# Kernel optimization log

Hardware: AMD Instinct MI355X
Metric: run time of the kernel (lower is better)

## Reference

```python
import jax, jax.numpy as jnp
import numpy as np
from jax import lax

NEG = -1e30  # finite stand-in for -inf (identical math through softmax/logaddexp, safe grads)


def _ctc_loss_sum(log_probs, labels, input_lens, label_lens, blank=0):
    """CTC negative log-likelihood, summed over batch (torch.nn.CTCLoss reduction='sum').
    log_probs: (T, B, V) log-softmaxed; labels: (B, L) int; lens: (B,) int."""
    T, B, V = log_probs.shape
    L = labels.shape[1]
    S = 2 * L + 1
    # extended label sequence with interleaved blanks: (B, S)
    ext = jnp.full((B, S), blank, dtype=labels.dtype).at[:, 1::2].set(labels)
    prev2 = jnp.concatenate([jnp.full((B, 2), blank, dtype=ext.dtype), ext[:, :-2]], axis=1)
    skip = (ext != blank) & (ext != prev2) & (jnp.arange(S)[None, :] >= 2)  # (B, S)
    # gather per-frame log-probs of extended labels: (T, B, S)
    lp_ext = log_probs[:, jnp.arange(B)[:, None], ext]
    alpha0 = jnp.full((B, S), NEG, log_probs.dtype)
    alpha0 = alpha0.at[:, 0].set(lp_ext[0, :, 0]).at[:, 1].set(lp_ext[0, :, 1])
    pad1 = jnp.full((B, 1), NEG, log_probs.dtype)
    pad2 = jnp.full((B, 2), NEG, log_probs.dtype)

    def step(alpha, inp):
        lp_t, t = inp
        a1 = jnp.concatenate([pad1, alpha[:, :-1]], axis=1)
        a2 = jnp.where(skip, jnp.concatenate([pad2, alpha[:, :-2]], axis=1), NEG)
        new = jnp.logaddexp(jnp.logaddexp(alpha, a1), a2) + lp_t
        new = jnp.where((t < input_lens)[:, None], new, alpha)  # freeze past each seq end
        return new, None

    alpha, _ = lax.scan(step, alpha0, (lp_ext[1:], jnp.arange(1, T)))
    bidx = jnp.arange(B)
    ll = jnp.logaddexp(alpha[bidx, 2 * label_lens - 1], alpha[bidx, 2 * label_lens])
    return -jnp.sum(ll)


def setup_inputs() -> dict:
    key = jax.random.key(0)
    k1, k2, k3 = jax.random.split(key, 3)
    B, T, D, V, L = 16, 1024, 512, 5000, 64
    hs_pad = jax.random.normal(k1, (B, T, D), dtype=jnp.float32)
    W = jax.random.normal(k2, (D, V), dtype=jnp.float32) * 0.02
    b = jnp.zeros((V,), dtype=jnp.float32)
    hlens = jnp.full((B,), T, dtype=jnp.int32)
    ys_pad = jax.random.randint(k3, (B, L), 1, V, dtype=jnp.int64)  # avoid blank id 0
    ys_lens = jnp.full((B,), L, dtype=jnp.int32)
    return {"hs_pad": hs_pad, "W": W, "b": b, "hlens": hlens, "ys_pad": ys_pad, "ys_lens": ys_lens}


def reference(hs_pad, W, b, hlens, ys_pad, ys_lens):
    B, T, D = hs_pad.shape
    V = W.shape[1]
    # ctc_lo projection (dropout_rate = 0.0 -> identity dropout)
    logits = jnp.einsum('btd,dv->btv', hs_pad, W) + b  # (B, T, V)
    # scatter-based mask: only classes appearing in ys_pad[b] plus ids {0,1} stay live
    allowed = jnp.zeros((B, V), dtype=bool)
    allowed = allowed.at[jnp.arange(B)[:, None], ys_pad].set(True).at[:, :2].set(True)
    logits = jnp.where(allowed[:, None, :], logits, NEG)  # masked_fill(-inf)
    log_probs = jax.nn.log_softmax(logits, axis=-1).transpose(1, 0, 2)  # (T, B, V)
    loss = _ctc_loss_sum(log_probs, ys_pad, hlens, ys_lens) / B
    return loss
```

## Files before the change

kernel.cpp:

```cpp
#include <hip/hip_runtime.h>
#include <hip/hip_bf16.h>
#include <cstdint>

#define NEGV -1e30f

constexpr int B = 16, T = 1024, D = 512, V = 5000, L = 64;
constexpr int NJ = 66;
constexpr int NJP = 80;
#define LOG2E 1.4426950408889634f
#define LN2   0.6931471805599453f
#define PSH   6.0f

typedef __attribute__((ext_vector_type(8))) short bf16x8;
typedef __attribute__((ext_vector_type(4))) int   i32x4;
typedef __attribute__((ext_vector_type(4))) float f32x4;

template <int CTRL>
__device__ __forceinline__ float dppf(float x) {
    return __int_as_float(__builtin_amdgcn_update_dpp(
        __float_as_int(x), __float_as_int(x), CTRL, 0xf, 0xf, false));
}
__device__ __forceinline__ float shup1(float x, float fill) {
    int r = __builtin_amdgcn_update_dpp(__float_as_int(fill), __float_as_int(x),
                                        0x138, 0xf, 0xf, false);
    return __int_as_float(r);
}
__device__ __forceinline__ float wmax64(float x) {
    x = fmaxf(x, dppf<0x111>(x));
    x = fmaxf(x, dppf<0x112>(x));
    x = fmaxf(x, dppf<0x114>(x));
    x = fmaxf(x, dppf<0x118>(x));
    x = fmaxf(x, dppf<0x142>(x));
    x = fmaxf(x, dppf<0x143>(x));
    return __int_as_float(__builtin_amdgcn_readlane(__float_as_int(x), 63));
}
__device__ __forceinline__ void ctc_step2(float& aA, float& aB, float& aE,
        float p_b, float p_l, float cpl) {
    float pA = shup1(aA, 0.f);
    float pB = shup1(aB, 0.f);
    float tS = aA + aB;
    float tA = aA * p_b;
    float tE = aE * p_b;
    float tP = pA * cpl;
    float nA = fmaf(pB, p_b, tA);
    float nB = fmaf(tS, p_l, tP);
    float nE = fmaf(aB, p_b, tE);
    aA = nA; aB = nB; aE = nE;
}
__device__ __forceinline__ void ctc_step2_g(float& aA, float& aB, float& aE,
        float p_b, float p_l, float cpl, bool upd) {
    float pA = shup1(aA, 0.f);
    float pB = shup1(aB, 0.f);
    float tS = aA + aB;
    float tA = aA * p_b;
    float tE = aE * p_b;
    float tP = pA * cpl;
    float nA = fmaf(pB, p_b, tA);
    float nB = fmaf(tS, p_l, tP);
    float nE = fmaf(aB, p_b, tE);
    if (upd) { aA = nA; aB = nB; aE = nE; }
}
__device__ __forceinline__ void renorm(float& x0, float& x1, float& x2, int& Esum) {
    float m = wmax64(fmaxf(fmaxf(x0, x1), x2));
    int e = ((__float_as_int(m) >> 23) & 255) - 127;
    float sc = __int_as_float((127 - e) << 23);
    x0 *= sc; x1 *= sc; x2 *= sc; Esum += e;
}
__device__ __forceinline__ int pk2(float lo, float hi) {
    return (int)((__float_as_uint(hi) & 0xFFFF0000u) | (__float_as_uint(lo) >> 16));
}

__global__ __launch_bounds__(256) void k_gather(const float* __restrict__ W,
        const float* __restrict__ bias, const int* __restrict__ ys,
        short* __restrict__ WgtT, float* __restrict__ biasG,
        unsigned* __restrict__ foMask) {
    int b = blockIdx.x, c = blockIdx.y, tid = threadIdx.x;
    __shared__ int cls[NJP];
    __shared__ unsigned mw[3];
    if (tid < NJP) cls[tid] = (tid < 2) ? tid : (tid < NJ ? ys[b * L + tid - 2] : 0);
    if (tid < 3) mw[tid] = 0u;
    __syncthreads();
    if (c == 0) {
        if (tid < NJ) {
            bool first = true;
            for (int k = 0; k < tid; ++k) if (cls[k] == cls[tid]) { first = false; break; }
            if (first) atomicOr(&mw[tid >> 5], 1u << (tid & 31));
        }
        __syncthreads();
        if (tid < 3) foMask[b * 4 + tid] = mw[tid];
        if (tid == 3) foMask[b * 4 + 3] = 0u;
        if (tid < NJP) biasG[b * NJP + tid] = (tid < NJ) ? bias[cls[tid]] : 0.f;
    }
    int kt = tid & 63, jg = tid >> 6;
    for (int j = jg; j < NJP; j += 4) {
        int d = c * 64 + kt;
        float v = (j < NJ) ? W[(size_t)d * V + cls[j]] : 0.f;
        WgtT[((size_t)b * NJP + j) * D + d] = (short)(__float_as_uint(v) >> 16);
    }
}

__global__ __launch_bounds__(64) void k_scores(const float* __restrict__ hs,
        const short* __restrict__ WgtT, const float* __restrict__ biasG,
        const unsigned* __restrict__ foMask,
        float* __restrict__ lpb, float* __restrict__ lplT) {
    int b = blockIdx.y, t0 = blockIdx.x * 16;
    int lane = threadIdx.x, cl = lane & 15, kg = lane >> 4;

    f32x4 acc[5];
    const float* __restrict__ bg = biasG + b * NJP;
    #pragma unroll
    for (int nt = 0; nt < 5; ++nt) {
        float bv = bg[nt * 16 + cl];
        acc[nt] = (f32x4){bv, bv, bv, bv};
    }

    const float* __restrict__ arow = hs + ((size_t)(b * T) + t0 + cl) * D + kg * 8;
    const short* __restrict__ brow = WgtT + ((size_t)b * NJP + cl) * D + kg * 8;

    #pragma unroll 4
    for (int ks = 0; ks < 16; ++ks) {
        int k0 = ks * 32;
        float4 a0 = *(const float4*)(arow + k0);
        float4 a1 = *(const float4*)(arow + k0 + 4);
        i32x4 ap = { pk2(a0.x, a0.y), pk2(a0.z, a0.w),
                     pk2(a1.x, a1.y), pk2(a1.z, a1.w) };
        bf16x8 af = __builtin_bit_cast(bf16x8, ap);
        #pragma unroll
        for (int nt = 0; nt < 5; ++nt) {
            bf16x8 bf = *(const bf16x8*)(brow + (size_t)nt * 16 * D + k0);
            acc[nt] = __builtin_amdgcn_mfma_f32_16x16x32_bf16(af, bf, acc[nt], 0, 0, 0);
        }
    }

    unsigned m0 = foMask[b * 4 + 0], m1 = foMask[b * 4 + 1], m2 = foMask[b * 4 + 2];
    bool on[5];
    on[0] = (m0 >> cl) & 1;        on[1] = (m0 >> (16 + cl)) & 1;
    on[2] = (m1 >> cl) & 1;        on[3] = (m1 >> (16 + cl)) & 1;
    on[4] = (cl < 2) ? ((m2 >> cl) & 1) : false;

    float lse[4];
    #pragma unroll
    for (int r = 0; r < 4; ++r) {
        float mx = NEGV;
        #pragma unroll
        for (int nt = 0; nt < 5; ++nt) if (on[nt]) mx = fmaxf(mx, acc[nt][r]);
        mx = fmaxf(mx, __shfl_xor(mx, 1));
        mx = fmaxf(mx, __shfl_xor(mx, 2));
        mx = fmaxf(mx, __shfl_xor(mx, 4));
        mx = fmaxf(mx, __shfl_xor(mx, 8));
        float s = 0.f;
        #pragma unroll
        for (int nt = 0; nt < 5; ++nt) if (on[nt]) s += __expf(acc[nt][r] - mx);
        s += __shfl_xor(s, 1);
        s += __shfl_xor(s, 2);
        s += __shfl_xor(s, 4);
        s += __shfl_xor(s, 8);
        lse[r] = mx + __logf(s);
    }

    __shared__ float Pt2[64][20];
    __shared__ float Pb[16];
    #pragma unroll
    for (int nt = 0; nt < 5; ++nt) {
        int col = nt * 16 + cl;
        #pragma unroll
        for (int r = 0; r < 4; ++r) {
            int t = kg * 4 + r;
            float pv = exp2f((acc[nt][r] - lse[r]) * LOG2E + PSH);
            if (col == 0) Pb[t] = pv;
            else if (col >= 2 && col < NJ) Pt2[col - 2][t] = pv;
        }
    }
    __syncthreads();
    float* __restrict__ orow = lplT + (size_t)b * 64 * T + (size_t)lane * T + t0;
    #pragma unroll
    for (int i = 0; i < 4; ++i)
        *(float4*)(orow + 4 * i) = *(const float4*)&Pt2[lane][4 * i];
    if (lane < 4) {
        float4 v = make_float4(Pb[4*lane], Pb[4*lane+1], Pb[4*lane+2], Pb[4*lane+3]);
        *(float4*)(lpb + b * T + t0 + 4 * lane) = v;
    }
}

__global__ __launch_bounds__(64) void k_ctc(const float* __restrict__ lpb,
        const float* __restrict__ lplT, const int* __restrict__ ys,
        const int* __restrict__ hlens, const int* __restrict__ yslens,
        float* __restrict__ ll) {
    int b = blockIdx.x, l = threadIdx.x;
    int lab = ys[b * L + l];
    int labm1 = __shfl_up(lab, 1);
    float skm = ((l >= 1) && (lab != 0) && (lab != labm1)) ? 1.0f : 0.0f;
    int hlen = hlens[b];
    int s2 = 2 * yslens[b];
    const float* __restrict__ lpbb = lpb + b * T;
    const float* __restrict__ lpt  = lplT + (size_t)b * 64 * T + (size_t)l * T;

    float aA = (l == 0) ? lpbb[0] : 0.f;
    float aB = (l == 0) ? lpt[0]  : 0.f;
    float aE = 0.f;
    int Esum = 0;

    float prl[15], prb[15];
    #pragma unroll
    for (int u = 0; u < 15; ++u) { prl[u] = lpt[1 + u]; prb[u] = lpbb[1 + u]; }
    float4 curl[4], curb[4], midl[4], midb[4], farl[4], farb[4];
    #pragma unroll
    for (int i = 0; i < 4; ++i) {
        curl[i] = *(const float4*)(lpt  + 16 + 4 * i);
        curb[i] = *(const float4*)(lpbb + 16 + 4 * i);
        midl[i] = *(const float4*)(lpt  + 32 + 4 * i);
        midb[i] = *(const float4*)(lpbb + 32 + 4 * i);
    }

    #pragma unroll
    for (int u = 0; u < 15; ++u) {
        int t = 1 + u;
        ctc_step2_g(aA, aB, aE, prb[u], prl[u], skm * prl[u], t < hlen);
    }
    renorm(aA, aB, aE, Esum);

    for (int g = 1; g < 64; ++g) {
        int t0 = 16 * g;
        if (g < 62) {
            const float* sl = lpt  + t0 + 32;
            const float* sb = lpbb + t0 + 32;
            #pragma unroll
            for (int i = 0; i < 4; ++i) {
                farl[i] = *(const float4*)(sl + 4 * i);
                farb[i] = *(const float4*)(sb + 4 * i);
            }
        }
        float pl[16], pb[16], cp[16];
        #pragma unroll
        for (int i = 0; i < 4; ++i) {
            pl[4*i+0] = curl[i].x; pl[4*i+1] = curl[i].y;
            pl[4*i+2] = curl[i].z; pl[4*i+3] = curl[i].w;
            pb[4*i+0] = curb[i].x; pb[4*i+1] = curb[i].y;
            pb[4*i+2] = curb[i].z; pb[4*i+3] = curb[i].w;
        }
        #pragma unroll
        for (int u = 0; u < 16; ++u) cp[u] = skm * pl[u];
        if (t0 + 16 <= hlen) {
            #pragma unroll
            for (int u = 0; u < 16; ++u)
                ctc_step2(aA, aB, aE, pb[u], pl[u], cp[u]);
        } else {
            #pragma unroll
            for (int u = 0; u < 16; ++u) {
                int t = t0 + u;
                ctc_step2_g(aA, aB, aE, pb[u], pl[u], cp[u], t < hlen);
            }
        }
        if ((g & 1) == 0 || g == 63) renorm(aA, aB, aE, Esum);
        #pragma unroll
        for (int i = 0; i < 4; ++i) {
            curl[i] = midl[i]; midl[i] = farl[i];
            curb[i] = midb[i]; midb[i] = farb[i];
        }
    }

    int s1 = s2 - 1;
    float v1 = __shfl(aB, s1 >> 1);
    float v2 = (s2 >= 2 * L) ? __shfl(aE, 63) : __shfl(aA, s2 >> 1);
    if (l == 0)
        ll[b] = LN2 * (__log2f(v1 + v2) + (float)Esum - PSH * (float)hlen);
}

__global__ void k_final(const float* __restrict__ ll, float* __restrict__ out) {
    if (threadIdx.x == 0 && blockIdx.x == 0) {
        float s = 0.f;
        for (int i = 0; i < B; ++i) s += ll[i];
        out[0] = -s / (float)B;
    }
}

extern "C" void kernel_launch(void* const* d_in, const int* in_sizes, int n_in,
                              void* d_out, int out_size, void* d_ws, size_t ws_size,
                              hipStream_t stream) {
    const float* hs    = (const float*)d_in[0];
    const float* W     = (const float*)d_in[1];
    const float* bias  = (const float*)d_in[2];
    const int*  hlens  = (const int*)d_in[3];
    const int*  ys     = (const int*)d_in[4];
    const int*  yslens = (const int*)d_in[5];

    char* ws = (char*)d_ws;
    unsigned* foMask = (unsigned*)(ws);
    float* biasG = (float*)(ws + 256);
    short* WgtT  = (short*)(ws + 5376);
    float* lpb   = (float*)(ws + 1316096);
    float* lplT  = (float*)(ws + 1381632);
    float* ll    = (float*)(ws + 5575936);

    hipLaunchKernelGGL(k_gather, dim3(B, 8), dim3(256), 0, stream,
                       W, bias, ys, WgtT, biasG, foMask);
    hipLaunchKernelGGL(k_scores, dim3(T / 16, B), dim3(64), 0, stream,
                       hs, WgtT, biasG, foMask, lpb, lplT);
    hipLaunchKernelGGL(k_ctc, dim3(B), dim3(64), 0, stream,
                       lpb, lplT, ys, hlens, yslens, ll);
    hipLaunchKernelGGL(k_final, dim3(1), dim3(64), 0, stream, ll, (float*)d_out);
}
```

Measured before the change: 88.93 us.

## Double k_scores time tile to reuse B fragments and fold final reduction into atomics

k_scores now handles 32 time steps per block using two accumulator sets, so each loaded bf16 weight fragment feeds two MFMAs and the grid is halved. Separately, the k_final launch is removed: k_gather zeroes the output and k_ctc atomically adds each batch's scaled loss. This cuts weight-load traffic and one kernel launch, but doubles register pressure in k_scores, leaves fewer blocks to fill the GPU, and makes the sum order nondeterministic.

```diff
diff --git a/kernel.cpp b/kernel.cpp
--- a/kernel.cpp
+++ b/kernel.cpp
@@ -73,8 +73,9 @@
 __global__ __launch_bounds__(256) void k_gather(const float* __restrict__ W,
         const float* __restrict__ bias, const int* __restrict__ ys,
         short* __restrict__ WgtT, float* __restrict__ biasG,
-        unsigned* __restrict__ foMask) {
+        unsigned* __restrict__ foMask, float* __restrict__ out) {
     int b = blockIdx.x, c = blockIdx.y, tid = threadIdx.x;
+    if (b == 0 && c == 0 && tid == 0) out[0] = 0.f;
     __shared__ int cls[NJP];
     __shared__ unsigned mw[3];
     if (tid < NJP) cls[tid] = (tid < 2) ? tid : (tid < NJ ? ys[b * L + tid - 2] : 0);
@@ -103,32 +104,40 @@
         const short* __restrict__ WgtT, const float* __restrict__ biasG,
         const unsigned* __restrict__ foMask,
         float* __restrict__ lpb, float* __restrict__ lplT) {
-    int b = blockIdx.y, t0 = blockIdx.x * 16;
+    int b = blockIdx.y, t0 = blockIdx.x * 32;
     int lane = threadIdx.x, cl = lane & 15, kg = lane >> 4;
 
-    f32x4 acc[5];
+    f32x4 acc0[5], acc1[5];
     const float* __restrict__ bg = biasG + b * NJP;
     #pragma unroll
     for (int nt = 0; nt < 5; ++nt) {
         float bv = bg[nt * 16 + cl];
-        acc[nt] = (f32x4){bv, bv, bv, bv};
-    }
-
-    const float* __restrict__ arow = hs + ((size_t)(b * T) + t0 + cl) * D + kg * 8;
+        acc0[nt] = (f32x4){bv, bv, bv, bv};
+        acc1[nt] = (f32x4){bv, bv, bv, bv};
+    }
+
+    const float* __restrict__ arow0 = hs + ((size_t)(b * T) + t0 + cl) * D + kg * 8;
+    const float* __restrict__ arow1 = arow0 + (size_t)16 * D;
     const short* __restrict__ brow = WgtT + ((size_t)b * NJP + cl) * D + kg * 8;
 
     #pragma unroll 4
     for (int ks = 0; ks < 16; ++ks) {
         int k0 = ks * 32;
-        float4 a0 = *(const float4*)(arow + k0);
-        float4 a1 = *(const float4*)(arow + k0 + 4);
-        i32x4 ap = { pk2(a0.x, a0.y), pk2(a0.z, a0.w),
-                     pk2(a1.x, a1.y), pk2(a1.z, a1.w) };
-        bf16x8 af = __builtin_bit_cast(bf16x8, ap);
+        float4 a0 = *(const float4*)(arow0 + k0);
+        float4 a1 = *(const float4*)(arow0 + k0 + 4);
+        float4 a2 = *(const float4*)(arow1 + k0);
+        float4 a3 = *(const float4*)(arow1 + k0 + 4);
+        i32x4 ap0 = { pk2(a0.x, a0.y), pk2(a0.z, a0.w),
+                      pk2(a1.x, a1.y), pk2(a1.z, a1.w) };
+        i32x4 ap1 = { pk2(a2.x, a2.y), pk2(a2.z, a2.w),
+                      pk2(a3.x, a3.y), pk2(a3.z, a3.w) };
+        bf16x8 af0 = __builtin_bit_cast(bf16x8, ap0);
+        bf16x8 af1 = __builtin_bit_cast(bf16x8, ap1);
         #pragma unroll
         for (int nt = 0; nt < 5; ++nt) {
             bf16x8 bf = *(const bf16x8*)(brow + (size_t)nt * 16 * D + k0);
-            acc[nt] = __builtin_amdgcn_mfma_f32_16x16x32_bf16(af, bf, acc[nt], 0, 0, 0);
+            acc0[nt] = __builtin_amdgcn_mfma_f32_16x16x32_bf16(af0, bf, acc0[nt], 0, 0, 0);
+            acc1[nt] = __builtin_amdgcn_mfma_f32_16x16x32_bf16(af1, bf, acc1[nt], 0, 0, 0);
         }
     }
 
@@ -138,45 +147,56 @@
     on[2] = (m1 >> cl) & 1;        on[3] = (m1 >> (16 + cl)) & 1;
     on[4] = (cl < 2) ? ((m2 >> cl) & 1) : false;
 
-    float lse[4];
+    float lse0[4], lse1[4];
     #pragma unroll
     for (int r = 0; r < 4; ++r) {
-        float mx = NEGV;
-        #pragma unroll
-        for (int nt = 0; nt < 5; ++nt) if (on[nt]) mx = fmaxf(mx, acc[nt][r]);
-        mx = fmaxf(mx, __shfl_xor(mx, 1));
-        mx = fmaxf(mx, __shfl_xor(mx, 2));
-        mx = fmaxf(mx, __shfl_xor(mx, 4));
-        mx = fmaxf(mx, __shfl_xor(mx, 8));
-        float s = 0.f;
-        #pragma unroll
-        for (int nt = 0; nt < 5; ++nt) if (on[nt]) s += __expf(acc[nt][r] - mx);
-        s += __shfl_xor(s, 1);
-        s += __shfl_xor(s, 2);
-        s += __shfl_xor(s, 4);
-        s += __shfl_xor(s, 8);
-        lse[r] = mx + __logf(s);
-    }
-
-    __shared__ float Pt2[64][20];
-    __shared__ float Pb[16];
+        float mxa = NEGV, mxb = NEGV;
+        #pragma unroll
+        for (int nt = 0; nt < 5; ++nt) if (on[nt]) {
+            mxa = fmaxf(mxa, acc0[nt][r]);
+            mxb = fmaxf(mxb, acc1[nt][r]);
+        }
+        mxa = fmaxf(mxa, __shfl_xor(mxa, 1)); mxb = fmaxf(mxb, __shfl_xor(mxb, 1));
+        mxa = fmaxf(mxa, __shfl_xor(mxa, 2)); mxb = fmaxf(mxb, __shfl_xor(mxb, 2));
+        mxa = fmaxf(mxa, __shfl_xor(mxa, 4)); mxb = fmaxf(mxb, __shfl_xor(mxb, 4));
+        mxa = fmaxf(mxa, __shfl_xor(mxa, 8)); mxb = fmaxf(mxb, __shfl_xor(mxb, 8));
+        float sa = 0.f, sb = 0.f;
+        #pragma unroll
+        for (int nt = 0; nt < 5; ++nt) if (on[nt]) {
+            sa += __expf(acc0[nt][r] - mxa);
+            sb += __expf(acc1[nt][r] - mxb);
+        }
+        sa += __shfl_xor(sa, 1); sb += __shfl_xor(sb, 1);
+        sa += __shfl_xor(sa, 2); sb += __shfl_xor(sb, 2);
+        sa += __shfl_xor(sa, 4); sb += __shfl_xor(sb, 4);
+        sa += __shfl_xor(sa, 8); sb += __shfl_xor(sb, 8);
+        lse0[r] = mxa + __logf(sa);
+        lse1[r] = mxb + __logf(sb);
+    }
+
+    __shared__ float Pt2[64][36];
+    __shared__ float Pb[32];
     #pragma unroll
     for (int nt = 0; nt < 5; ++nt) {
         int col = nt * 16 + cl;
         #pragma unroll
         for (int r = 0; r < 4; ++r) {
             int t = kg * 4 + r;
-            float pv = exp2f((acc[nt][r] - lse[r]) * LOG2E + PSH);
-            if (col == 0) Pb[t] = pv;
-            else if (col >= 2 && col < NJ) Pt2[col - 2][t] = pv;
+            float pv0 = exp2f((acc0[nt][r] - lse0[r]) * LOG2E + PSH);
+            float pv1 = exp2f((acc1[nt][r] - lse1[r]) * LOG2E + PSH);
+            if (col == 0) { Pb[t] = pv0; Pb[t + 16] = pv1; }
+            else if (col >= 2 && col < NJ) {
+                Pt2[col - 2][t] = pv0;
+                Pt2[col - 2][t + 16] = pv1;
+            }
         }
     }
     __syncthreads();
     float* __restrict__ orow = lplT + (size_t)b * 64 * T + (size_t)lane * T + t0;
     #pragma unroll
-    for (int i = 0; i < 4; ++i)
+    for (int i = 0; i < 8; ++i)
         *(float4*)(orow + 4 * i) = *(const float4*)&Pt2[lane][4 * i];
-    if (lane < 4) {
+    if (lane < 8) {
         float4 v = make_float4(Pb[4*lane], Pb[4*lane+1], Pb[4*lane+2], Pb[4*lane+3]);
         *(float4*)(lpb + b * T + t0 + 4 * lane) = v;
     }
@@ -185,7 +205,7 @@
 __global__ __launch_bounds__(64) void k_ctc(const float* __restrict__ lpb,
         const float* __restrict__ lplT, const int* __restrict__ ys,
         const int* __restrict__ hlens, const int* __restrict__ yslens,
-        float* __restrict__ ll) {
+        float* __restrict__ out) {
     int b = blockIdx.x, l = threadIdx.x;
     int lab = ys[b * L + l];
     int labm1 = __shfl_up(lab, 1);
@@ -262,15 +282,9 @@
     int s1 = s2 - 1;
     float v1 = __shfl(aB, s1 >> 1);
     float v2 = (s2 >= 2 * L) ? __shfl(aE, 63) : __shfl(aA, s2 >> 1);
-    if (l == 0)
-        ll[b] = LN2 * (__log2f(v1 + v2) + (float)Esum - PSH * (float)hlen);
-}
-
-__global__ void k_final(const float* __restrict__ ll, float* __restrict__ out) {
-    if (threadIdx.x == 0 && blockIdx.x == 0) {
-        float s = 0.f;
-        for (int i = 0; i < B; ++i) s += ll[i];
-        out[0] = -s / (float)B;
+    if (l == 0) {
+        float llb = LN2 * (__log2f(v1 + v2) + (float)Esum - PSH * (float)hlen);
+        atomicAdd(out, -llb * (1.0f / (float)B));
     }
 }
 
@@ -290,13 +304,11 @@
     short* WgtT  = (short*)(ws + 5376);
     float* lpb   = (float*)(ws + 1316096);
     float* lplT  = (float*)(ws + 1381632);
-    float* ll    = (float*)(ws + 5575936);
 
     hipLaunchKernelGGL(k_gather, dim3(B, 8), dim3(256), 0, stream,
-                       W, bias, ys, WgtT, biasG, foMask);
-    hipLaunchKernelGGL(k_scores, dim3(T / 16, B), dim3(64), 0, stream,
+                       W, bias, ys, WgtT, biasG, foMask, (float*)d_out);
+    hipLaunchKernelGGL(k_scores, dim3(T / 32, B), dim3(64), 0, stream,
                        hs, WgtT, biasG, foMask, lpb, lplT);
     hipLaunchKernelGGL(k_ctc, dim3(B), dim3(64), 0, stream,
-                       lpb, lplT, ys, hlens, yslens, ll);
-    hipLaunchKernelGGL(k_final, dim3(1), dim3(64), 0, stream, ll, (float*)d_out);
-}
+                       lpb, lplT, ys, hlens, yslens, (float*)d_out);
+}
```

Result: slower. 102.7 us (+15.5%).
